# Performance work log

Measured on AMD Instinct MI355X. Metric: run time of the kernel, lower is better.

## Reference

```python
import jax, jax.numpy as jnp
import numpy as np

DIM = 1024
N_HEAD = 16
HEAD_DIM = DIM // N_HEAD
B, T = 2, 2048


def setup_inputs() -> dict:
    key = jax.random.key(0)
    ks = jax.random.split(key, 9)
    s = 1.0 / np.sqrt(DIM)
    return {
        "x": jax.random.normal(ks[0], (B, T, DIM), dtype=jnp.float32),
        "Wq": jax.random.normal(ks[1], (DIM, DIM), dtype=jnp.float32) * s,
        "bq": jax.random.normal(ks[2], (DIM,), dtype=jnp.float32) * s,
        "Wk": jax.random.normal(ks[3], (DIM, DIM), dtype=jnp.float32) * s,
        "bk": jax.random.normal(ks[4], (DIM,), dtype=jnp.float32) * s,
        "Wv": jax.random.normal(ks[5], (DIM, DIM), dtype=jnp.float32) * s,
        "bv": jax.random.normal(ks[6], (DIM,), dtype=jnp.float32) * s,
        "Wo": jax.random.normal(ks[7], (DIM, DIM), dtype=jnp.float32) * s,
        "bo": jax.random.normal(ks[8], (DIM,), dtype=jnp.float32) * s,
    }


def reference(x, Wq, bq, Wk, bk, Wv, bv, Wo, bo):
    b, t, d = x.shape
    # torch nn.Linear: y = x @ W.T + b
    Q = x @ Wq.T + bq  # [b, t, d]
    K = x @ Wk.T + bk
    V = x @ Wv.T + bv
    # split heads -> [b, h, t, hd]
    Q = Q.reshape(b, t, N_HEAD, HEAD_DIM).transpose(0, 2, 1, 3)
    K = K.reshape(b, t, N_HEAD, HEAD_DIM).transpose(0, 2, 1, 3)
    V = V.reshape(b, t, N_HEAD, HEAD_DIM).transpose(0, 2, 1, 3)
    scale = 1.0 / jnp.sqrt(jnp.float32(HEAD_DIM))
    score = jnp.einsum('bhqd,bhkd->bhqk', Q, K) * scale  # [b, h, t, t]
    attn = jax.nn.softmax(score, axis=-1)
    # dropout is identity in eval mode
    out = jnp.einsum('bhqk,bhkd->bhqd', attn, V)  # [b, h, t, hd]
    out = out.transpose(0, 2, 1, 3).reshape(b, t, d)
    return out @ Wo.T + bo
```

## Files before the change

kernel.cpp:

```cpp
#include <hip/hip_runtime.h>


#define DIM 1024
#define NH 16
#define HD 64
#define SEQ 2048
#define NROWS 4096

typedef unsigned short u16;
typedef __bf16 bf16_t;
typedef bf16_t bf16x8 __attribute__((ext_vector_type(8)));
typedef float f32x4 __attribute__((ext_vector_type(4)));
typedef u16 u16x4 __attribute__((ext_vector_type(4)));

typedef const __attribute__((address_space(1))) void* gas_ptr;
typedef __attribute__((address_space(3))) void* las_ptr;

#define S_BARRIER() asm volatile("s_barrier" ::: "memory")
#define S_WAITCNT_VM(N) asm volatile("s_waitcnt vmcnt(" #N ")" ::: "memory")

__device__ __forceinline__ void gl_lds16(const void* g, void* lds_wave_base) {
  __builtin_amdgcn_global_load_lds((gas_ptr)g, (las_ptr)lds_wave_base, 16, 0, 0);
}

__device__ __forceinline__ f32x4 mfma_bf16(bf16x8 a, bf16x8 b, f32x4 c) {
  return __builtin_amdgcn_mfma_f32_16x16x32_bf16(a, b, c, 0, 0, 0);
}

__device__ __forceinline__ u16 bfu(float f) {
  bf16_t b = (bf16_t)f;
  union { bf16_t b; u16 u; } cv; cv.b = b; return cv.u;
}

__device__ __forceinline__ float fexp2(float x) {
#if __has_builtin(__builtin_amdgcn_exp2f)
  return __builtin_amdgcn_exp2f(x);
#else
  return exp2f(x);
#endif
}

#define QSCALE 0.18033688f

__global__ void cvt_x(const float* __restrict__ in, u16* __restrict__ out) {
  int i = blockIdx.x * 256 + threadIdx.x;
  float4 v = ((const float4*)in)[i];
  u16x4 o;
  o.x = bfu(v.x); o.y = bfu(v.y); o.z = bfu(v.z); o.w = bfu(v.w);
  ((u16x4*)out)[i] = o;
}

__global__ void cvt_w4(const float* __restrict__ wq, const float* __restrict__ wk,
                       const float* __restrict__ wv, const float* __restrict__ wo,
                       u16* __restrict__ oq, u16* __restrict__ ok,
                       u16* __restrict__ ov, u16* __restrict__ oo) {
  const int which = blockIdx.y;
  const float* in = which == 0 ? wq : which == 1 ? wk : which == 2 ? wv : wo;
  u16* out = which == 0 ? oq : which == 1 ? ok : which == 2 ? ov : oo;
  const float s = which == 0 ? QSCALE : 1.0f;
  int i = blockIdx.x * 256 + threadIdx.x;
  float4 v = ((const float4*)in)[i];
  u16x4 o;
  o.x = bfu(v.x * s); o.y = bfu(v.y * s); o.z = bfu(v.z * s); o.w = bfu(v.w * s);
  ((u16x4*)out)[i] = o;
}

__global__ __launch_bounds__(256, 3) void gemm_qkv(const u16* __restrict__ A,
                                                   const u16* __restrict__ wq,
                                                   const u16* __restrict__ wk,
                                                   const u16* __restrict__ wv,
                                                   const float* __restrict__ bq,
                                                   const float* __restrict__ bk,
                                                   const float* __restrict__ bv,
                                                   u16* __restrict__ Qb,
                                                   u16* __restrict__ Kb,
                                                   u16* __restrict__ Vtb) {
  __shared__ u16 As[2][128 * 32];
  __shared__ u16 Bs[2][128 * 32];
  const int which = blockIdx.x >> 3;
  const int col0 = (blockIdx.x & 7) * 128;
  const u16* W = which == 0 ? wq : which == 1 ? wk : wv;
  const float* bias = which == 0 ? bq : which == 1 ? bk : bv;
  const float bscale = which == 0 ? QSCALE : 1.0f;

  const int t = threadIdx.x, lane = t & 63, w = t >> 6;
  const int row0 = blockIdx.y * 128;
  const int wr = w >> 1, wc = w & 1;
  const int lr = lane & 15, lk = lane >> 4;

  f32x4 acc[4][4] = {};

  auto stage = [&](int k0, int bu) {
#pragma unroll
    for (int i = 0; i < 2; ++i) {
      const int bc = i * 256 + w * 64;
      const int f = bc + lane;
      gl_lds16(A + (size_t)(row0 + (f >> 2)) * DIM + k0 + (f & 3) * 8, &As[bu][bc * 8]);
      gl_lds16(W + (size_t)(col0 + (f >> 2)) * DIM + k0 + (f & 3) * 8, &Bs[bu][bc * 8]);
    }
  };

  stage(0, 0);
  int buf = 0;
  for (int k0 = 0; k0 < DIM; k0 += 32) {
    if (k0 + 32 < DIM) { stage(k0 + 32, buf ^ 1); S_WAITCNT_VM(4); }
    else               { S_WAITCNT_VM(0); }
    S_BARRIER();

    bf16x8 a[4], b[4];
#pragma unroll
    for (int m = 0; m < 4; ++m)
      a[m] = *(const bf16x8*)&As[buf][(wr * 64 + m * 16 + lr) * 32 + lk * 8];
#pragma unroll
    for (int n = 0; n < 4; ++n)
      b[n] = *(const bf16x8*)&Bs[buf][(wc * 64 + n * 16 + lr) * 32 + lk * 8];
    __builtin_amdgcn_s_setprio(1);
#pragma unroll
    for (int m = 0; m < 4; ++m)
#pragma unroll
      for (int n = 0; n < 4; ++n)
        acc[m][n] = mfma_bf16(a[m], b[n], acc[m][n]);
    __builtin_amdgcn_s_setprio(0);

    S_BARRIER();
    buf ^= 1;
  }

#pragma unroll
  for (int m = 0; m < 4; ++m) {
    const int rowb = row0 + wr * 64 + m * 16 + lk * 4;
#pragma unroll
    for (int n = 0; n < 4; ++n) {
      const int ocol = col0 + wc * 64 + n * 16 + lr;
      const float bc = bias[ocol] * bscale;
#pragma unroll
      for (int r = 0; r < 4; ++r) {
        const int rr = rowb + r;
        const float v = acc[m][n][r] + bc;
        if (which == 0) {
          Qb[(size_t)rr * DIM + ocol] = bfu(v);
        } else if (which == 1) {
          Kb[(size_t)rr * DIM + ocol] = bfu(v);
        } else {
          const size_t idx = ((((size_t)(rr >> 11) * NH + (ocol >> 6)) * HD + (ocol & 63)) << 11) + (rr & 2047);
          Vtb[idx] = bfu(v);
        }
      }
    }
  }
}

__global__ __launch_bounds__(256, 3) void gemm_out(const u16* __restrict__ A,
                                                   const u16* __restrict__ W,
                                                   const float* __restrict__ bias,
                                                   float* __restrict__ C) {
  __shared__ u16 As[2][128 * 32];
  __shared__ u16 Bs[2][128 * 32];
  const int t = threadIdx.x, lane = t & 63, w = t >> 6;
  const int row0 = blockIdx.y * 128, col0 = blockIdx.x * 128;
  const int wr = w >> 1, wc = w & 1;
  const int lr = lane & 15, lk = lane >> 4;

  f32x4 acc[4][4] = {};

  auto stage = [&](int k0, int bu) {
#pragma unroll
    for (int i = 0; i < 2; ++i) {
      const int bc = i * 256 + w * 64;
      const int f = bc + lane;
      gl_lds16(A + (size_t)(row0 + (f >> 2)) * DIM + k0 + (f & 3) * 8, &As[bu][bc * 8]);
      gl_lds16(W + (size_t)(col0 + (f >> 2)) * DIM + k0 + (f & 3) * 8, &Bs[bu][bc * 8]);
    }
  };

  stage(0, 0);
  int buf = 0;
  for (int k0 = 0; k0 < DIM; k0 += 32) {
    if (k0 + 32 < DIM) { stage(k0 + 32, buf ^ 1); S_WAITCNT_VM(4); }
    else               { S_WAITCNT_VM(0); }
    S_BARRIER();

    bf16x8 a[4], b[4];
#pragma unroll
    for (int m = 0; m < 4; ++m)
      a[m] = *(const bf16x8*)&As[buf][(wr * 64 + m * 16 + lr) * 32 + lk * 8];
#pragma unroll
    for (int n = 0; n < 4; ++n)
      b[n] = *(const bf16x8*)&Bs[buf][(wc * 64 + n * 16 + lr) * 32 + lk * 8];
    __builtin_amdgcn_s_setprio(1);
#pragma unroll
    for (int m = 0; m < 4; ++m)
#pragma unroll
      for (int n = 0; n < 4; ++n)
        acc[m][n] = mfma_bf16(a[m], b[n], acc[m][n]);
    __builtin_amdgcn_s_setprio(0);

    S_BARRIER();
    buf ^= 1;
  }

#pragma unroll
  for (int m = 0; m < 4; ++m) {
    const int rowb = row0 + wr * 64 + m * 16 + lk * 4;
#pragma unroll
    for (int n = 0; n < 4; ++n) {
      const int col = col0 + wc * 64 + n * 16 + lr;
      const float bc = bias[col];
#pragma unroll
      for (int r = 0; r < 4; ++r)
        C[(size_t)(rowb + r) * DIM + col] = acc[m][n][r] + bc;
    }
  }
}

__global__ __launch_bounds__(256, 4) void flash_attn(const u16* __restrict__ Q,
                                                     const u16* __restrict__ K,
                                                     const u16* __restrict__ Vt,
                                                     u16* __restrict__ O) {
  __shared__ u16 Ks[2][64 * 64];
  __shared__ u16 Vs[2][64 * 64];
  __shared__ u16 Ps[4][16][64];

  const int t = threadIdx.x, lane = t & 63, w = t >> 6;
  const int L = blockIdx.x;
  const int bh = ((L >> 8) << 3) | (L & 7);
  const int qt = (L >> 3) & 31;
  const int b = bh >> 4, h = bh & 15;
  const int q0 = qt * 64;
  const int lr = lane & 15, lk = lane >> 4;

  const size_t qrow = (size_t)(b * SEQ + q0 + w * 16 + lr);
  bf16x8 qf[2];
  qf[0] = *(const bf16x8*)&Q[qrow * DIM + h * HD + lk * 8];
  qf[1] = *(const bf16x8*)&Q[qrow * DIM + h * HD + lk * 8 + 32];

  f32x4 o[4] = {};
  float m0 = -INFINITY, l0 = 0.f;

  auto stage = [&](int kt, int bu) {
#pragma unroll
    for (int i = 0; i < 2; ++i) {
      const int bc = i * 256 + w * 64;
      const int f = bc + lane;
      const int row = f >> 3, c = f & 7;
      const int cs = c ^ (row & 7);
      gl_lds16(K + (size_t)(b * SEQ + kt + row) * DIM + h * HD + cs * 8, &Ks[bu][bc * 8]);
      gl_lds16(Vt + (((size_t)bh * HD + row) << 11) + kt + cs * 8, &Vs[bu][bc * 8]);
    }
  };

  stage(0, 0);
  int buf = 0;
  for (int kt = 0; kt < SEQ; kt += 64) {
    if (kt + 64 < SEQ) { stage(kt + 64, buf ^ 1); S_WAITCNT_VM(4); }
    else               { S_WAITCNT_VM(0); }
    S_BARRIER();

    const u16* ks = Ks[buf];
    const u16* vs = Vs[buf];

    f32x4 s[4] = {};
    __builtin_amdgcn_s_setprio(1);
#pragma unroll
    for (int n = 0; n < 4; ++n) {
      const int row = n * 16 + lr;
#pragma unroll
      for (int kk = 0; kk < 2; ++kk) {
        bf16x8 kf = *(const bf16x8*)&ks[row * 64 + (((lk + kk * 4) ^ (row & 7)) * 8)];
        s[n] = mfma_bf16(kf, qf[kk], s[n]);
      }
    }
    __builtin_amdgcn_s_setprio(0);

    f32x4 m4 = s[0];
#pragma unroll
    for (int n = 1; n < 4; ++n) {
      m4[0] = fmaxf(m4[0], s[n][0]); m4[1] = fmaxf(m4[1], s[n][1]);
      m4[2] = fmaxf(m4[2], s[n][2]); m4[3] = fmaxf(m4[3], s[n][3]);
    }
    float mx = fmaxf(fmaxf(m4[0], m4[1]), fmaxf(m4[2], m4[3]));
    mx = fmaxf(mx, __shfl_xor(mx, 16));
    mx = fmaxf(mx, __shfl_xor(mx, 32));
    if (__any(mx > m0 + 8.0f)) {
      const float mnew = fmaxf(m0, mx);
      const float alpha = fexp2(m0 - mnew);
      m0 = mnew;
      l0 *= alpha;
#pragma unroll
      for (int r = 0; r < 4; ++r) {
        const float a_r = __shfl(alpha, lk * 4 + r);
#pragma unroll
        for (int nd = 0; nd < 4; ++nd) o[nd][r] *= a_r;
      }
    }

    float p[4][4];
    float rs = 0.f;
#pragma unroll
    for (int n = 0; n < 4; ++n)
#pragma unroll
      for (int r = 0; r < 4; ++r) { p[n][r] = fexp2(s[n][r] - m0); rs += p[n][r]; }
    rs += __shfl_xor(rs, 16);
    rs += __shfl_xor(rs, 32);
    l0 += rs;

    const int rx = (lr & 7) << 3;
#pragma unroll
    for (int n = 0; n < 4; ++n) {
      u16x4 pk;
      pk.x = bfu(p[n][0]); pk.y = bfu(p[n][1]); pk.z = bfu(p[n][2]); pk.w = bfu(p[n][3]);
      *(u16x4*)&Ps[w][lr][(n * 16 + lk * 4) ^ rx] = pk;
    }

    __builtin_amdgcn_s_setprio(1);
#pragma unroll
    for (int kk = 0; kk < 2; ++kk) {
      bf16x8 pa = *(const bf16x8*)&Ps[w][lr][(kk * 32 + lk * 8) ^ rx];
#pragma unroll
      for (int nd = 0; nd < 4; ++nd) {
        const int vrow = nd * 16 + lr;
        bf16x8 vf = *(const bf16x8*)&vs[vrow * 64 + (((lk + kk * 4) ^ (vrow & 7)) * 8)];
        o[nd] = mfma_bf16(pa, vf, o[nd]);
      }
    }
    __builtin_amdgcn_s_setprio(0);

    S_BARRIER();
    buf ^= 1;
  }

#pragma unroll
  for (int r = 0; r < 4; ++r) {
    const float inv = 1.f / __shfl(l0, lk * 4 + r);
    const size_t grow = (size_t)(b * SEQ + q0 + w * 16 + lk * 4 + r);
#pragma unroll
    for (int nd = 0; nd < 4; ++nd)
      O[grow * DIM + h * HD + nd * 16 + lr] = bfu(o[nd][r] * inv);
  }
}

extern "C" void kernel_launch(void* const* d_in, const int* in_sizes, int n_in,
                              void* d_out, int out_size, void* d_ws, size_t ws_size,
                              hipStream_t stream) {
  (void)in_sizes; (void)n_in; (void)out_size; (void)ws_size;
  const float* x  = (const float*)d_in[0];
  const float* Wq = (const float*)d_in[1];
  const float* bq = (const float*)d_in[2];
  const float* Wk = (const float*)d_in[3];
  const float* bk = (const float*)d_in[4];
  const float* Wv = (const float*)d_in[5];
  const float* bv = (const float*)d_in[6];
  const float* Wo = (const float*)d_in[7];
  const float* bo = (const float*)d_in[8];

  char* ws = (char*)d_ws;
  u16* xb  = (u16*)(ws + 0);
  u16* wqb = (u16*)(ws + 8388608);
  u16* wkb = (u16*)(ws + 10485760);
  u16* wvb = (u16*)(ws + 12582912);
  u16* wob = (u16*)(ws + 14680064);
  u16* Qb  = (u16*)(ws + 16777216);
  u16* Kb  = (u16*)(ws + 25165824);
  u16* Vtb = (u16*)(ws + 33554432);
  u16* Ob  = (u16*)(ws + 41943040);

  cvt_x<<<NROWS * DIM / 4 / 256, 256, 0, stream>>>(x, xb);
  cvt_w4<<<dim3(DIM * DIM / 4 / 256, 4), 256, 0, stream>>>(Wq, Wk, Wv, Wo, wqb, wkb, wvb, wob);

  gemm_qkv<<<dim3(24, NROWS / 128), 256, 0, stream>>>(xb, wqb, wkb, wvb, bq, bk, bv, Qb, Kb, Vtb);

  flash_attn<<<1024, 256, 0, stream>>>(Qb, Kb, Vtb, Ob);

  gemm_out<<<dim3(DIM / 128, NROWS / 128), 256, 0, stream>>>(Ob, wob, bo, (float*)d_out);
}
```

Baseline: 138.3 us.

## Keep softmax probabilities in registers for PV MFMA and swizzle GEMM blocks across XCDs

```diff
diff --git a/kernel.cpp b/kernel.cpp
--- a/kernel.cpp
+++ b/kernel.cpp
@@ -8,10 +8,13 @@
 #define NROWS 4096
 
 typedef unsigned short u16;
+typedef unsigned int u32;
 typedef __bf16 bf16_t;
 typedef bf16_t bf16x8 __attribute__((ext_vector_type(8)));
 typedef float f32x4 __attribute__((ext_vector_type(4)));
 typedef u16 u16x4 __attribute__((ext_vector_type(4)));
+typedef short i16x4 __attribute__((ext_vector_type(4)));
+typedef u32 u32x2 __attribute__((ext_vector_type(2)));
 
 typedef const __attribute__((address_space(1))) void* gas_ptr;
 typedef __attribute__((address_space(3))) void* las_ptr;
@@ -25,6 +28,21 @@
 
 __device__ __forceinline__ f32x4 mfma_bf16(bf16x8 a, bf16x8 b, f32x4 c) {
   return __builtin_amdgcn_mfma_f32_16x16x32_bf16(a, b, c, 0, 0, 0);
+}
+
+__device__ __forceinline__ f32x4 mfma16_bf16(i16x4 a, i16x4 b, f32x4 c) {
+#if __has_builtin(__builtin_amdgcn_mfma_f32_16x16x16bf16_1k)
+  return __builtin_amdgcn_mfma_f32_16x16x16bf16_1k(a, b, c, 0, 0, 0);
+#else
+  asm("v_mfma_f32_16x16x16_bf16 %0, %1, %2, %0" : "+v"(c) : "v"(a), "v"(b));
+  return c;
+#endif
+}
+
+__device__ __forceinline__ u32 cvtpk(float lo, float hi) {
+  u32 r;
+  asm("v_cvt_pk_bf16_f32 %0, %1, %2" : "=v"(r) : "v"(lo), "v"(hi));
+  return r;
 }
 
 __device__ __forceinline__ u16 bfu(float f) {
@@ -65,6 +83,10 @@
   ((u16x4*)out)[i] = o;
 }
 
+__device__ __forceinline__ int xcd_swz(int L, int nwg) {
+  return (L & 7) * (nwg >> 3) + (L >> 3);
+}
+
 __global__ __launch_bounds__(256, 3) void gemm_qkv(const u16* __restrict__ A,
                                                    const u16* __restrict__ wq,
                                                    const u16* __restrict__ wk,
@@ -77,14 +99,17 @@
                                                    u16* __restrict__ Vtb) {
   __shared__ u16 As[2][128 * 32];
   __shared__ u16 Bs[2][128 * 32];
-  const int which = blockIdx.x >> 3;
-  const int col0 = (blockIdx.x & 7) * 128;
+  const int L = blockIdx.y * gridDim.x + blockIdx.x;
+  const int swz = xcd_swz(L, gridDim.x * gridDim.y);
+  const int bx = swz % gridDim.x, by = swz / gridDim.x;
+  const int which = bx >> 3;
+  const int col0 = (bx & 7) * 128;
   const u16* W = which == 0 ? wq : which == 1 ? wk : wv;
   const float* bias = which == 0 ? bq : which == 1 ? bk : bv;
   const float bscale = which == 0 ? QSCALE : 1.0f;
 
   const int t = threadIdx.x, lane = t & 63, w = t >> 6;
-  const int row0 = blockIdx.y * 128;
+  const int row0 = by * 128;
   const int wr = w >> 1, wc = w & 1;
   const int lr = lane & 15, lk = lane >> 4;
 
@@ -156,8 +181,11 @@
                                                    float* __restrict__ C) {
   __shared__ u16 As[2][128 * 32];
   __shared__ u16 Bs[2][128 * 32];
+  const int L = blockIdx.y * gridDim.x + blockIdx.x;
+  const int swz = xcd_swz(L, gridDim.x * gridDim.y);
+  const int bx = swz % gridDim.x, by = swz / gridDim.x;
   const int t = threadIdx.x, lane = t & 63, w = t >> 6;
-  const int row0 = blockIdx.y * 128, col0 = blockIdx.x * 128;
+  const int row0 = by * 128, col0 = bx * 128;
   const int wr = w >> 1, wc = w & 1;
   const int lr = lane & 15, lk = lane >> 4;
 
@@ -213,13 +241,12 @@
   }
 }
 
-__global__ __launch_bounds__(256, 4) void flash_attn(const u16* __restrict__ Q,
+__global__ __launch_bounds__(256, 5) void flash_attn(const u16* __restrict__ Q,
                                                      const u16* __restrict__ K,
                                                      const u16* __restrict__ Vt,
                                                      u16* __restrict__ O) {
   __shared__ u16 Ks[2][64 * 64];
   __shared__ u16 Vs[2][64 * 64];
-  __shared__ u16 Ps[4][16][64];
 
   const int t = threadIdx.x, lane = t & 63, w = t >> 6;
   const int L = blockIdx.x;
@@ -304,23 +331,24 @@
     rs += __shfl_xor(rs, 32);
     l0 += rs;
 
-    const int rx = (lr & 7) << 3;
+    i16x4 paf[4];
 #pragma unroll
     for (int n = 0; n < 4; ++n) {
-      u16x4 pk;
-      pk.x = bfu(p[n][0]); pk.y = bfu(p[n][1]); pk.z = bfu(p[n][2]); pk.w = bfu(p[n][3]);
-      *(u16x4*)&Ps[w][lr][(n * 16 + lk * 4) ^ rx] = pk;
+      u32x2 pk;
+      pk[0] = cvtpk(p[n][0], p[n][1]);
+      pk[1] = cvtpk(p[n][2], p[n][3]);
+      paf[n] = __builtin_bit_cast(i16x4, pk);
     }
 
     __builtin_amdgcn_s_setprio(1);
 #pragma unroll
-    for (int kk = 0; kk < 2; ++kk) {
-      bf16x8 pa = *(const bf16x8*)&Ps[w][lr][(kk * 32 + lk * 8) ^ rx];
+    for (int n = 0; n < 4; ++n) {
 #pragma unroll
       for (int nd = 0; nd < 4; ++nd) {
         const int vrow = nd * 16 + lr;
-        bf16x8 vf = *(const bf16x8*)&vs[vrow * 64 + (((lk + kk * 4) ^ (vrow & 7)) * 8)];
-        o[nd] = mfma_bf16(pa, vf, o[nd]);
+        const int chunk = (2 * n + (lk >> 1)) ^ (vrow & 7);
+        i16x4 vb = *(const i16x4*)&vs[vrow * 64 + chunk * 8 + (lk & 1) * 4];
+        o[nd] = mfma16_bf16(paf[n], vb, o[nd]);
       }
     }
     __builtin_amdgcn_s_setprio(0);
```

Result: no change. 139.5 us (+0.9%).
